# Kernel optimization log

Measured on AMD Instinct MI355X. Metric: run time of the kernel, lower is better.

The kernel has to match this reference:

```python
import jax, jax.numpy as jnp
import numpy as np

T, H = 4096, 2048

def setup_inputs() -> dict:
    key = jax.random.key(0)
    k1, k2, k3 = jax.random.split(key, 3)
    x_sequence = jax.random.normal(k1, (T, H), dtype=jnp.float32)
    lamda = jax.random.normal(k2, (H,), dtype=jnp.float32) * 0.2
    B = jax.random.normal(k3, (H, H), dtype=jnp.float32) / jnp.sqrt(jnp.float32(H))
    return {"x_sequence": x_sequence, "lamda": lamda, "B": B}

def reference(x_sequence, lamda, B):
    # h_t = lamda \odot h_{t-1} + B @ x_t ; initial h_0 = 0 (reset_rtrl_state).
    # Returns stacked h over all T steps, matching torch.stack(outputs).
    def step(h, x_t):
        h_next = lamda * h + B @ x_t  # [H]
        return h_next, h_next
    h0 = jnp.zeros_like(lamda)
    _, hs = jax.lax.scan(step, h0, x_sequence)  # hs: [T, H]
    return hs
```

## Files before the change

kernel.cpp:

```cpp
#include <hip/hip_runtime.h>
#include <hip/hip_bf16.h>

#define T_DIM 4096
#define H_DIM 2048
#define K_DIM 2048
#define NCHUNK 64
#define CLEN 64
#define NT (K_DIM / 64)

typedef float f32x4 __attribute__((ext_vector_type(4)));
typedef _Float16 f16x8 __attribute__((ext_vector_type(8)));

typedef const __attribute__((address_space(1))) char* gp1;
typedef __attribute__((address_space(3))) char* lp3;

static const size_t nX = (size_t)T_DIM * K_DIM;
static const size_t nB = (size_t)H_DIM * K_DIM;

__global__ __launch_bounds__(256) void cvt_swz_all(const float* __restrict__ X,
                                                   const float* __restrict__ Bm,
                                                   _Float16* __restrict__ Xh,
                                                   _Float16* __restrict__ Bh) {
    size_t i = ((size_t)blockIdx.x * 256 + threadIdx.x) * 8;
    const float* in;
    _Float16* out;
    size_t j;
    if (i < nX) { in = X;  out = Xh; j = i; }
    else        { in = Bm; out = Bh; j = i - nX; }
    int row  = (int)(j >> 11);
    int colB = (int)(j & 2047) * 2;
    float a[8];
    *(f32x4*)(a)     = *(const f32x4*)(in + j);
    *(f32x4*)(a + 4) = *(const f32x4*)(in + j + 4);
    f16x8 h;
#pragma unroll
    for (int k = 0; k < 8; ++k) h[k] = (_Float16)a[k];
    size_t ob = (size_t)row * 4096 + (size_t)(colB ^ ((row & 7) << 4));
    *(f16x8*)((char*)out + ob) = h;
}

__global__ __launch_bounds__(512, 4) void gemm_f16(const _Float16* __restrict__ Xh,
                                                   const _Float16* __restrict__ Bh,
                                                   const float* __restrict__ lamda,
                                                   _Float16* __restrict__ Yh,
                                                   float* __restrict__ e) {
    __shared__ __align__(16) _Float16 sMem[2][2][128 * 64];

    int bid = blockIdx.x;
    int swz = (bid & 7) * 64 + (bid >> 3);
    const int h0 = (swz & 15) * 128;
    const int t0 = (swz >> 4) * 128;

    const int tid  = threadIdx.x;
    const int lane = tid & 63;
    const int wave = tid >> 6;
    const int wrow = (wave >> 2) & 1;
    const int wcol = (wave >> 1) & 1;
    const int kks  = wave & 1;
    const int ln15 = lane & 15;
    const int kq   = lane >> 4;

    f32x4 acc[4][4] = {};

    const int srow = tid >> 3;
    const int kcB  = (tid & 7) * 16;
    size_t gA0[2], gB0[2];
    unsigned ldsOff[2];
#pragma unroll
    for (int q = 0; q < 2; ++q) {
        gA0[q] = (size_t)(t0 + srow + q * 64) * 4096 + kcB;
        gB0[q] = (size_t)(h0 + srow + q * 64) * 4096 + kcB;
        ldsOff[q] = (unsigned)(q * 8192 + wave * 1024);
    }

    const int kb = kks * 64 + kq * 16;
    int offA[4], offB[4];
#pragma unroll
    for (int m = 0; m < 4; ++m) {
        int rA = wrow * 64 + m * 16 + ln15;
        offA[m] = rA * 128 + (kb ^ ((rA & 7) << 4));
        int rB = wcol * 64 + m * 16 + ln15;
        offB[m] = rB * 128 + (kb ^ ((rB & 7) << 4));
    }

#define STAGE(buf, kt)                                                                   \
    {                                                                                    \
        _Pragma("unroll")                                                                \
        for (int q = 0; q < 2; ++q) {                                                    \
            __builtin_amdgcn_global_load_lds((gp1)((const char*)Xh + gA0[q] + (kt) * 128), \
                                             (lp3)((char*)sMem[buf][0] + ldsOff[q]), 16, 0, 0); \
            __builtin_amdgcn_global_load_lds((gp1)((const char*)Bh + gB0[q] + (kt) * 128), \
                                             (lp3)((char*)sMem[buf][1] + ldsOff[q]), 16, 0, 0); \
        }                                                                                \
    }

#define COMPUTE(buf)                                                                     \
    {                                                                                    \
        const char* pA = (const char*)sMem[buf][0];                                      \
        const char* pB = (const char*)sMem[buf][1];                                      \
        f16x8 fa[4], fb[4];                                                              \
        _Pragma("unroll")                                                                \
        for (int m = 0; m < 4; ++m) fa[m] = *(const f16x8*)(pA + offA[m]);               \
        _Pragma("unroll")                                                                \
        for (int n = 0; n < 4; ++n) fb[n] = *(const f16x8*)(pB + offB[n]);               \
        _Pragma("unroll")                                                                \
        for (int m = 0; m < 4; ++m)                                                      \
            _Pragma("unroll")                                                            \
            for (int n = 0; n < 4; ++n)                                                  \
                acc[m][n] = __builtin_amdgcn_mfma_f32_16x16x32_f16(fa[m], fb[n],         \
                                                                  acc[m][n], 0, 0, 0);  \
    }

    STAGE(0, 0);
    __syncthreads();

    int cur = 0;
    for (int kt = 0; kt < NT; ++kt) {
        if (kt + 1 < NT) STAGE(cur ^ 1, kt + 1);
        COMPUTE(cur);
        __syncthreads();
        cur ^= 1;
    }
#undef STAGE
#undef COMPUTE

    const int p = wrow * 2 + wcol;
    float* red = (float*)sMem;
    if (kks == 1) {
#pragma unroll
        for (int m = 0; m < 4; ++m)
#pragma unroll
            for (int n = 0; n < 4; ++n)
                *(f32x4*)((char*)red + p * 16384 + (m * 4 + n) * 1024 + lane * 16) = acc[m][n];
    }
    __syncthreads();
    if (kks == 0) {
#pragma unroll
        for (int m = 0; m < 4; ++m)
#pragma unroll
            for (int n = 0; n < 4; ++n)
                acc[m][n] += *(const f32x4*)((const char*)red + p * 16384 + (m * 4 + n) * 1024 + lane * 16);

#pragma unroll
        for (int m = 0; m < 4; ++m) {
            int row = t0 + wrow * 64 + m * 16 + kq * 4;
#pragma unroll
            for (int n = 0; n < 4; ++n) {
                int col = h0 + wcol * 64 + n * 16 + ln15;
#pragma unroll
                for (int j = 0; j < 4; ++j)
                    Yh[(size_t)(row + j) * H_DIM + col] = (_Float16)acc[m][n][j];
            }
        }

        const int c = (t0 >> 6) + wrow;
#pragma unroll
        for (int n = 0; n < 4; ++n) {
            int col = h0 + wcol * 64 + n * 16 + ln15;
            float lam  = lamda[col];
            float lam2 = lam * lam;
            float lam4 = lam2 * lam2;
            float lam16 = lam4 * lam4 * lam4 * lam4;
            float hsum = 0.f;
#pragma unroll
            for (int m = 0; m < 4; ++m) {
                float hm = fmaf(fmaf(fmaf(acc[m][n][0], lam, acc[m][n][1]), lam,
                                     acc[m][n][2]), lam, acc[m][n][3]);
                hsum = fmaf(hsum, lam16, hm);
            }
            float w = 1.f;
            if (kq < 3) w = lam4;
            if (kq < 2) w *= lam4;
            if (kq < 1) w *= lam4;
            float T = hsum * w;
            T += __shfl_xor(T, 16);
            T += __shfl_xor(T, 32);
            if (kq == 0) e[(size_t)c * H_DIM + col] = T;
        }
    }
}

__global__ __launch_bounds__(256) void scanCB(const _Float16* __restrict__ Yh,
                                              float* __restrict__ Y,
                                              const float* __restrict__ lamda,
                                              const float* __restrict__ e) {
    int c = blockIdx.x >> 3;
    int h = (blockIdx.x & 7) * 256 + threadIdx.x;
    float lam = lamda[h];
    float lamL = lam;
#pragma unroll
    for (int i = 0; i < 6; ++i) lamL *= lamL;
    float s = 0.f;
    for (int ci = 0; ci < c; ++ci)
        s = fmaf(lamL, s, e[(size_t)ci * H_DIM + h]);
    const _Float16* qi = Yh + (size_t)c * CLEN * H_DIM + h;
    float* qo = Y + (size_t)c * CLEN * H_DIM + h;
#pragma unroll
    for (int t = 0; t < CLEN; ++t) {
        float v = fmaf(lam, s, (float)qi[(size_t)t * H_DIM]);
        qo[(size_t)t * H_DIM] = v;
        s = v;
    }
}

__global__ __launch_bounds__(256) void gemm_xbT_split(const float* __restrict__ X,
                                                      const float* __restrict__ Bm,
                                                      float* __restrict__ Y) {
    __shared__ __align__(16) _Float16 Ah[128 * 64];
    __shared__ __align__(16) _Float16 Al[128 * 64];
    __shared__ __align__(16) _Float16 Bh2[128 * 64];
    __shared__ __align__(16) _Float16 Bl[128 * 64];

    const int tid  = threadIdx.x;
    const int t0   = blockIdx.y * 128;
    const int h0   = blockIdx.x * 128;
    const int lane = tid & 63;
    const int wave = tid >> 6;
    const int wrow = wave >> 1;
    const int wcol = wave & 1;
    const int ln15 = lane & 15;
    const int kq   = lane >> 4;

    f32x4 acc[4][4] = {};

    int baseA[4], swzA[4], baseB[4], swzB[4];
#pragma unroll
    for (int m = 0; m < 4; ++m) {
        int rA = wrow * 64 + m * 16 + ln15;
        baseA[m] = rA * 128; swzA[m] = (rA & 7) << 4;
        int rB = wcol * 64 + m * 16 + ln15;
        baseB[m] = rB * 128; swzB[m] = (rB & 7) << 4;
    }

    for (int kt = 0; kt < NT; ++kt) {
        const int k0 = kt * 64;
        __syncthreads();
#pragma unroll
        for (int t = 0; t < 4; ++t) {
            int cc  = tid + t * 256;
            int row = cc >> 3;
            int kc  = (cc & 7) * 8;
            size_t gA = (size_t)(t0 + row) * K_DIM + k0 + kc;
            size_t gB = (size_t)(h0 + row) * K_DIM + k0 + kc;
            float a[8], b[8];
            *(float4*)(a)     = *(const float4*)(X + gA);
            *(float4*)(a + 4) = *(const float4*)(X + gA + 4);
            *(float4*)(b)     = *(const float4*)(Bm + gB);
            *(float4*)(b + 4) = *(const float4*)(Bm + gB + 4);
            f16x8 ah, al, bh, bl;
#pragma unroll
            for (int j = 0; j < 8; ++j) {
                _Float16 hh = (_Float16)a[j];
                ah[j] = hh; al[j] = (_Float16)(a[j] - (float)hh);
                _Float16 gg = (_Float16)b[j];
                bh[j] = gg; bl[j] = (_Float16)(b[j] - (float)gg);
            }
            int off = row * 128 + ((kc * 2) ^ ((row & 7) << 4));
            *(f16x8*)((char*)Ah + off)  = ah;
            *(f16x8*)((char*)Al + off)  = al;
            *(f16x8*)((char*)Bh2 + off) = bh;
            *(f16x8*)((char*)Bl + off)  = bl;
        }
        __syncthreads();
#pragma unroll
        for (int kk = 0; kk < 2; ++kk) {
            const int kb2 = kk * 64 + kq * 16;
            f16x8 fa[4], fb[4], ft[4];
#pragma unroll
            for (int m = 0; m < 4; ++m)
                fa[m] = *(const f16x8*)((const char*)Ah + baseA[m] + (kb2 ^ swzA[m]));
#pragma unroll
            for (int m = 0; m < 4; ++m)
                fb[m] = *(const f16x8*)((const char*)Bh2 + baseB[m] + (kb2 ^ swzB[m]));
#pragma unroll
            for (int m = 0; m < 4; ++m)
#pragma unroll
                for (int n = 0; n < 4; ++n)
                    acc[m][n] = __builtin_amdgcn_mfma_f32_16x16x32_f16(fa[m], fb[n], acc[m][n], 0, 0, 0);
#pragma unroll
            for (int m = 0; m < 4; ++m)
                ft[m] = *(const f16x8*)((const char*)Bl + baseB[m] + (kb2 ^ swzB[m]));
#pragma unroll
            for (int m = 0; m < 4; ++m)
#pragma unroll
                for (int n = 0; n < 4; ++n)
                    acc[m][n] = __builtin_amdgcn_mfma_f32_16x16x32_f16(fa[m], ft[n], acc[m][n], 0, 0, 0);
#pragma unroll
            for (int m = 0; m < 4; ++m)
                ft[m] = *(const f16x8*)((const char*)Al + baseA[m] + (kb2 ^ swzA[m]));
#pragma unroll
            for (int m = 0; m < 4; ++m)
#pragma unroll
                for (int n = 0; n < 4; ++n)
                    acc[m][n] = __builtin_amdgcn_mfma_f32_16x16x32_f16(ft[m], fb[n], acc[m][n], 0, 0, 0);
        }
    }

#pragma unroll
    for (int m = 0; m < 4; ++m) {
        int row = t0 + wrow * 64 + m * 16 + kq * 4;
#pragma unroll
        for (int n = 0; n < 4; ++n) {
            int col = h0 + wcol * 64 + n * 16 + ln15;
#pragma unroll
            for (int j = 0; j < 4; ++j)
                Y[(size_t)(row + j) * H_DIM + col] = acc[m][n][j];
        }
    }
}

__global__ __launch_bounds__(256) void scanA(const float* __restrict__ Y,
                                             const float* __restrict__ lamda,
                                             float* __restrict__ e) {
    int c = blockIdx.x >> 3;
    int h = (blockIdx.x & 7) * 256 + threadIdx.x;
    float lam = lamda[h];
    float s = 0.f;
    const float* p = Y + (size_t)c * CLEN * H_DIM + h;
#pragma unroll
    for (int t = 0; t < CLEN; ++t) { s = fmaf(lam, s, *p); p += H_DIM; }
    e[(size_t)c * H_DIM + h] = s;
}

__global__ __launch_bounds__(256) void scanCB_plain(float* __restrict__ Y,
                                                    const float* __restrict__ lamda,
                                                    const float* __restrict__ e) {
    int c = blockIdx.x >> 3;
    int h = (blockIdx.x & 7) * 256 + threadIdx.x;
    float lam = lamda[h];
    float lamL = lam;
#pragma unroll
    for (int i = 0; i < 6; ++i) lamL *= lamL;
    float s = 0.f;
    for (int ci = 0; ci < c; ++ci)
        s = fmaf(lamL, s, e[(size_t)ci * H_DIM + h]);
    float* q = Y + (size_t)c * CLEN * H_DIM + h;
#pragma unroll
    for (int t = 0; t < CLEN; ++t) {
        float v = fmaf(lam, s, q[(size_t)t * H_DIM]);
        q[(size_t)t * H_DIM] = v;
        s = v;
    }
}

extern "C" void kernel_launch(void* const* d_in, const int* in_sizes, int n_in,
                              void* d_out, int out_size, void* d_ws, size_t ws_size,
                              hipStream_t stream) {
    const float* X   = (const float*)d_in[0];
    const float* lam = (const float*)d_in[1];
    const float* Bm  = (const float*)d_in[2];
    float* Y = (float*)d_out;

    const size_t needFused = (2 * nX + nB) * sizeof(_Float16)
                           + (size_t)NCHUNK * H_DIM * sizeof(float);

    if (ws_size >= needFused) {
        _Float16* Xh = (_Float16*)d_ws;
        _Float16* Bh = Xh + nX;
        _Float16* Yh = Bh + nB;
        float* e = (float*)(Yh + nX);

        int cvtBlocks = (int)((nX + nB) / 8 / 256);
        cvt_swz_all<<<dim3(cvtBlocks), 256, 0, stream>>>(X, Bm, Xh, Bh);
        gemm_f16<<<dim3(512), 512, 0, stream>>>(Xh, Bh, lam, Yh, e);
        scanCB<<<dim3(NCHUNK * 8), 256, 0, stream>>>(Yh, Y, lam, e);
    } else {
        dim3 grid(H_DIM / 128, T_DIM / 128);
        gemm_xbT_split<<<grid, 256, 0, stream>>>(X, Bm, Y);
        float* e = (float*)d_ws;
        scanA<<<dim3(NCHUNK * 8), 256, 0, stream>>>(Y, lam, e);
        scanCB_plain<<<dim3(NCHUNK * 8), 256, 0, stream>>>(Y, lam, e);
    }
}
```

Before: 72.94 us.

## Add split-K 256x256-tile GEMM path with dual partial outputs summed in scan

Adds a new GEMM kernel that uses 256x256 output tiles and splits K in two, giving 256 blocks, each writing its own fp16 partial Y and chunk-end state. The scan kernel then sums both partials while it runs the recurrence. Larger tiles raise arithmetic intensity and split-K keeps enough blocks in flight. In exchange it needs extra workspace, writes and reads an additional fp16 Y buffer, and rounds each partial to fp16 before the sum. The old fp32 split fallback path is removed, so small workspaces no longer launch anything.

```diff
diff --git a/kernel.cpp b/kernel.cpp
--- a/kernel.cpp
+++ b/kernel.cpp
@@ -6,7 +6,6 @@
 #define K_DIM 2048
 #define NCHUNK 64
 #define CLEN 64
-#define NT (K_DIM / 64)
 
 typedef float f32x4 __attribute__((ext_vector_type(4)));
 typedef _Float16 f16x8 __attribute__((ext_vector_type(8)));
@@ -39,6 +38,175 @@
     *(f16x8*)((char*)out + ob) = h;
 }
 
+__global__ __launch_bounds__(512, 2) void gemm_sk(const _Float16* __restrict__ Xh,
+                                                  const _Float16* __restrict__ Bh,
+                                                  const float* __restrict__ lamda,
+                                                  _Float16* __restrict__ Yh0,
+                                                  _Float16* __restrict__ Yh1,
+                                                  float* __restrict__ e0,
+                                                  float* __restrict__ e1) {
+    __shared__ __align__(16) _Float16 sA[2][256 * 64];
+    __shared__ __align__(16) _Float16 sB[2][256 * 64];
+
+    const int bid = blockIdx.x;
+    const int x  = bid & 7;
+    const int jj = bid >> 3;
+    const int kz = x >> 2;
+    const int q  = x & 3;
+    const int t0 = (q * 4 + (jj >> 3)) * 256;
+    const int h0 = (jj & 7) * 256;
+    _Float16* __restrict__ Yh = kz ? Yh1 : Yh0;
+    float* __restrict__ e     = kz ? e1 : e0;
+
+    const int tid  = threadIdx.x;
+    const int lane = tid & 63;
+    const int wave = tid >> 6;
+    const int wrow = wave >> 2;
+    const int wcol = wave & 3;
+    const int ln15 = lane & 15;
+    const int kq   = lane >> 4;
+
+    f32x4 acc[8][4] = {};
+
+    size_t gA0[4], gB0[4];
+    unsigned ldsOff[4];
+#pragma unroll
+    for (int t = 0; t < 4; ++t) {
+        int s   = tid + t * 512;
+        int row = s >> 3;
+        int kc  = (s & 7) * 16;
+        gA0[t] = (size_t)(t0 + row) * 4096 + (size_t)(kz * 2048) + kc;
+        gB0[t] = (size_t)(h0 + row) * 4096 + (size_t)(kz * 2048) + kc;
+        ldsOff[t] = (unsigned)((t * 512 + wave * 64) * 16);
+    }
+
+    int baseA[8], swzA[8], baseB[4], swzB[4];
+#pragma unroll
+    for (int m = 0; m < 8; ++m) {
+        int rA = wrow * 128 + m * 16 + ln15;
+        baseA[m] = rA * 128; swzA[m] = (rA & 7) << 4;
+    }
+#pragma unroll
+    for (int n = 0; n < 4; ++n) {
+        int rB = wcol * 64 + n * 16 + ln15;
+        baseB[n] = rB * 128; swzB[n] = (rB & 7) << 4;
+    }
+
+#define STAGE(buf, kt)                                                                   \
+    {                                                                                    \
+        _Pragma("unroll")                                                                \
+        for (int t = 0; t < 4; ++t) {                                                    \
+            __builtin_amdgcn_global_load_lds((gp1)((const char*)Xh + gA0[t] + (kt) * 128), \
+                                             (lp3)((char*)sA[buf] + ldsOff[t]), 16, 0, 0); \
+            __builtin_amdgcn_global_load_lds((gp1)((const char*)Bh + gB0[t] + (kt) * 128), \
+                                             (lp3)((char*)sB[buf] + ldsOff[t]), 16, 0, 0); \
+        }                                                                                \
+    }
+
+#define COMPUTE(buf)                                                                     \
+    {                                                                                    \
+        const char* pA = (const char*)sA[buf];                                           \
+        const char* pB = (const char*)sB[buf];                                           \
+        _Pragma("unroll")                                                                \
+        for (int kk = 0; kk < 2; ++kk) {                                                 \
+            const int kb = kk * 64 + kq * 16;                                            \
+            f16x8 fa[8], fb[4];                                                          \
+            _Pragma("unroll")                                                            \
+            for (int m = 0; m < 8; ++m)                                                  \
+                fa[m] = *(const f16x8*)(pA + baseA[m] + (kb ^ swzA[m]));                 \
+            _Pragma("unroll")                                                            \
+            for (int n = 0; n < 4; ++n)                                                  \
+                fb[n] = *(const f16x8*)(pB + baseB[n] + (kb ^ swzB[n]));                 \
+            _Pragma("unroll")                                                            \
+            for (int m = 0; m < 8; ++m)                                                  \
+                _Pragma("unroll")                                                        \
+                for (int n = 0; n < 4; ++n)                                              \
+                    acc[m][n] = __builtin_amdgcn_mfma_f32_16x16x32_f16(fa[m], fb[n],     \
+                                                                      acc[m][n], 0, 0, 0); \
+        }                                                                                \
+    }
+
+    STAGE(0, 0);
+    __syncthreads();
+
+    int cur = 0;
+    for (int kt = 0; kt < 16; ++kt) {
+        if (kt + 1 < 16) STAGE(cur ^ 1, kt + 1);
+        COMPUTE(cur);
+        __syncthreads();
+        cur ^= 1;
+    }
+#undef STAGE
+#undef COMPUTE
+
+#pragma unroll
+    for (int m = 0; m < 8; ++m) {
+        int row = t0 + wrow * 128 + m * 16 + kq * 4;
+#pragma unroll
+        for (int n = 0; n < 4; ++n) {
+            int col = h0 + wcol * 64 + n * 16 + ln15;
+#pragma unroll
+            for (int j2 = 0; j2 < 4; ++j2)
+                Yh[(size_t)(row + j2) * H_DIM + col] = (_Float16)acc[m][n][j2];
+        }
+    }
+
+#pragma unroll
+    for (int half = 0; half < 2; ++half) {
+        const int c = (t0 >> 6) + wrow * 2 + half;
+#pragma unroll
+        for (int n = 0; n < 4; ++n) {
+            int col = h0 + wcol * 64 + n * 16 + ln15;
+            float lam  = lamda[col];
+            float lam2 = lam * lam;
+            float lam4 = lam2 * lam2;
+            float lam16 = lam4 * lam4 * lam4 * lam4;
+            float hsum = 0.f;
+#pragma unroll
+            for (int mm = 0; mm < 4; ++mm) {
+                int m = half * 4 + mm;
+                float hm = fmaf(fmaf(fmaf(acc[m][n][0], lam, acc[m][n][1]), lam,
+                                     acc[m][n][2]), lam, acc[m][n][3]);
+                hsum = fmaf(hsum, lam16, hm);
+            }
+            float w = 1.f;
+            if (kq < 3) w = lam4;
+            if (kq < 2) w *= lam4;
+            if (kq < 1) w *= lam4;
+            float T = hsum * w;
+            T += __shfl_xor(T, 16);
+            T += __shfl_xor(T, 32);
+            if (kq == 0) e[(size_t)c * H_DIM + col] = T;
+        }
+    }
+}
+
+__global__ __launch_bounds__(256) void scanCB_sk(const _Float16* __restrict__ Yh0,
+                                                 const _Float16* __restrict__ Yh1,
+                                                 float* __restrict__ Y,
+                                                 const float* __restrict__ lamda,
+                                                 const float* __restrict__ e0,
+                                                 const float* __restrict__ e1) {
+    int c = blockIdx.x >> 3;
+    int h = (blockIdx.x & 7) * 256 + threadIdx.x;
+    float lam = lamda[h];
+    float lamL = lam;
+#pragma unroll
+    for (int i = 0; i < 6; ++i) lamL *= lamL;
+    float s = 0.f;
+    for (int ci = 0; ci < c; ++ci)
+        s = fmaf(lamL, s, e0[(size_t)ci * H_DIM + h] + e1[(size_t)ci * H_DIM + h]);
+    const _Float16* q0 = Yh0 + (size_t)c * CLEN * H_DIM + h;
+    const _Float16* q1 = Yh1 + (size_t)c * CLEN * H_DIM + h;
+    float* qo = Y + (size_t)c * CLEN * H_DIM + h;
+#pragma unroll
+    for (int t = 0; t < CLEN; ++t) {
+        float v = fmaf(lam, s, (float)q0[(size_t)t * H_DIM] + (float)q1[(size_t)t * H_DIM]);
+        qo[(size_t)t * H_DIM] = v;
+        s = v;
+    }
+}
+
 __global__ __launch_bounds__(512, 4) void gemm_f16(const _Float16* __restrict__ Xh,
                                                    const _Float16* __restrict__ Bh,
                                                    const float* __restrict__ lamda,
@@ -115,8 +283,8 @@
     __syncthreads();
 
     int cur = 0;
-    for (int kt = 0; kt < NT; ++kt) {
-        if (kt + 1 < NT) STAGE(cur ^ 1, kt + 1);
+    for (int kt = 0; kt < K_DIM / 64; ++kt) {
+        if (kt + 1 < K_DIM / 64) STAGE(cur ^ 1, kt + 1);
         COMPUTE(cur);
         __syncthreads();
         cur ^= 1;
@@ -180,10 +348,10 @@
     }
 }
 
-__global__ __launch_bounds__(256) void scanCB(const _Float16* __restrict__ Yh,
-                                              float* __restrict__ Y,
-                                              const float* __restrict__ lamda,
-                                              const float* __restrict__ e) {
+__global__ __launch_bounds__(256) void scanCB_f16(const _Float16* __restrict__ Yh,
+                                                  float* __restrict__ Y,
+                                                  const float* __restrict__ lamda,
+                                                  const float* __restrict__ e) {
     int c = blockIdx.x >> 3;
     int h = (blockIdx.x & 7) * 256 + threadIdx.x;
     float lam = lamda[h];
@@ -199,146 +367,6 @@
     for (int t = 0; t < CLEN; ++t) {
         float v = fmaf(lam, s, (float)qi[(size_t)t * H_DIM]);
         qo[(size_t)t * H_DIM] = v;
-        s = v;
-    }
-}
-
-__global__ __launch_bounds__(256) void gemm_xbT_split(const float* __restrict__ X,
-                                                      const float* __restrict__ Bm,
-                                                      float* __restrict__ Y) {
-    __shared__ __align__(16) _Float16 Ah[128 * 64];
-    __shared__ __align__(16) _Float16 Al[128 * 64];
-    __shared__ __align__(16) _Float16 Bh2[128 * 64];
-    __shared__ __align__(16) _Float16 Bl[128 * 64];
-
-    const int tid  = threadIdx.x;
-    const int t0   = blockIdx.y * 128;
-    const int h0   = blockIdx.x * 128;
-    const int lane = tid & 63;
-    const int wave = tid >> 6;
-    const int wrow = wave >> 1;
-    const int wcol = wave & 1;
-    const int ln15 = lane & 15;
-    const int kq   = lane >> 4;
-
-    f32x4 acc[4][4] = {};
-
-    int baseA[4], swzA[4], baseB[4], swzB[4];
-#pragma unroll
-    for (int m = 0; m < 4; ++m) {
-        int rA = wrow * 64 + m * 16 + ln15;
-        baseA[m] = rA * 128; swzA[m] = (rA & 7) << 4;
-        int rB = wcol * 64 + m * 16 + ln15;
-        baseB[m] = rB * 128; swzB[m] = (rB & 7) << 4;
-    }
-
-    for (int kt = 0; kt < NT; ++kt) {
-        const int k0 = kt * 64;
-        __syncthreads();
-#pragma unroll
-        for (int t = 0; t < 4; ++t) {
-            int cc  = tid + t * 256;
-            int row = cc >> 3;
-            int kc  = (cc & 7) * 8;
-            size_t gA = (size_t)(t0 + row) * K_DIM + k0 + kc;
-            size_t gB = (size_t)(h0 + row) * K_DIM + k0 + kc;
-            float a[8], b[8];
-            *(float4*)(a)     = *(const float4*)(X + gA);
-            *(float4*)(a + 4) = *(const float4*)(X + gA + 4);
-            *(float4*)(b)     = *(const float4*)(Bm + gB);
-            *(float4*)(b + 4) = *(const float4*)(Bm + gB + 4);
-            f16x8 ah, al, bh, bl;
-#pragma unroll
-            for (int j = 0; j < 8; ++j) {
-                _Float16 hh = (_Float16)a[j];
-                ah[j] = hh; al[j] = (_Float16)(a[j] - (float)hh);
-                _Float16 gg = (_Float16)b[j];
-                bh[j] = gg; bl[j] = (_Float16)(b[j] - (float)gg);
-            }
-            int off = row * 128 + ((kc * 2) ^ ((row & 7) << 4));
-            *(f16x8*)((char*)Ah + off)  = ah;
-            *(f16x8*)((char*)Al + off)  = al;
-            *(f16x8*)((char*)Bh2 + off) = bh;
-            *(f16x8*)((char*)Bl + off)  = bl;
-        }
-        __syncthreads();
-#pragma unroll
-        for (int kk = 0; kk < 2; ++kk) {
-            const int kb2 = kk * 64 + kq * 16;
-            f16x8 fa[4], fb[4], ft[4];
-#pragma unroll
-            for (int m = 0; m < 4; ++m)
-                fa[m] = *(const f16x8*)((const char*)Ah + baseA[m] + (kb2 ^ swzA[m]));
-#pragma unroll
-            for (int m = 0; m < 4; ++m)
-                fb[m] = *(const f16x8*)((const char*)Bh2 + baseB[m] + (kb2 ^ swzB[m]));
-#pragma unroll
-            for (int m = 0; m < 4; ++m)
-#pragma unroll
-                for (int n = 0; n < 4; ++n)
-                    acc[m][n] = __builtin_amdgcn_mfma_f32_16x16x32_f16(fa[m], fb[n], acc[m][n], 0, 0, 0);
-#pragma unroll
-            for (int m = 0; m < 4; ++m)
-                ft[m] = *(const f16x8*)((const char*)Bl + baseB[m] + (kb2 ^ swzB[m]));
-#pragma unroll
-            for (int m = 0; m < 4; ++m)
-#pragma unroll
-                for (int n = 0; n < 4; ++n)
-                    acc[m][n] = __builtin_amdgcn_mfma_f32_16x16x32_f16(fa[m], ft[n], acc[m][n], 0, 0, 0);
-#pragma unroll
-            for (int m = 0; m < 4; ++m)
-                ft[m] = *(const f16x8*)((const char*)Al + baseA[m] + (kb2 ^ swzA[m]));
-#pragma unroll
-            for (int m = 0; m < 4; ++m)
-#pragma unroll
-                for (int n = 0; n < 4; ++n)
-                    acc[m][n] = __builtin_amdgcn_mfma_f32_16x16x32_f16(ft[m], fb[n], acc[m][n], 0, 0, 0);
-        }
-    }
-
-#pragma unroll
-    for (int m = 0; m < 4; ++m) {
-        int row = t0 + wrow * 64 + m * 16 + kq * 4;
-#pragma unroll
-        for (int n = 0; n < 4; ++n) {
-            int col = h0 + wcol * 64 + n * 16 + ln15;
-#pragma unroll
-            for (int j = 0; j < 4; ++j)
-                Y[(size_t)(row + j) * H_DIM + col] = acc[m][n][j];
-        }
-    }
-}
-
-__global__ __launch_bounds__(256) void scanA(const float* __restrict__ Y,
-                                             const float* __restrict__ lamda,
-                                             float* __restrict__ e) {
-    int c = blockIdx.x >> 3;
-    int h = (blockIdx.x & 7) * 256 + threadIdx.x;
-    float lam = lamda[h];
-    float s = 0.f;
-    const float* p = Y + (size_t)c * CLEN * H_DIM + h;
-#pragma unroll
-    for (int t = 0; t < CLEN; ++t) { s = fmaf(lam, s, *p); p += H_DIM; }
-    e[(size_t)c * H_DIM + h] = s;
-}
-
-__global__ __launch_bounds__(256) void scanCB_plain(float* __restrict__ Y,
-                                                    const float* __restrict__ lamda,
-                                                    const float* __restrict__ e) {
-    int c = blockIdx.x >> 3;
-    int h = (blockIdx.x & 7) * 256 + threadIdx.x;
-    float lam = lamda[h];
-    float lamL = lam;
-#pragma unroll
-    for (int i = 0; i < 6; ++i) lamL *= lamL;
-    float s = 0.f;
-    for (int ci = 0; ci < c; ++ci)
-        s = fmaf(lamL, s, e[(size_t)ci * H_DIM + h]);
-    float* q = Y + (size_t)c * CLEN * H_DIM + h;
-#pragma unroll
-    for (int t = 0; t < CLEN; ++t) {
-        float v = fmaf(lam, s, q[(size_t)t * H_DIM]);
-        q[(size_t)t * H_DIM] = v;
         s = v;
     }
 }
@@ -351,24 +379,32 @@
     const float* Bm  = (const float*)d_in[2];
     float* Y = (float*)d_out;
 
-    const size_t needFused = (2 * nX + nB) * sizeof(_Float16)
-                           + (size_t)NCHUNK * H_DIM * sizeof(float);
-
-    if (ws_size >= needFused) {
+    const size_t needSK  = (3 * nX + nB) * sizeof(_Float16)
+                         + 2ull * NCHUNK * H_DIM * sizeof(float);
+    const size_t needR14 = (2 * nX + nB) * sizeof(_Float16)
+                         + (size_t)NCHUNK * H_DIM * sizeof(float);
+
+    int cvtBlocks = (int)((nX + nB) / 8 / 256);
+
+    if (ws_size >= needSK) {
+        _Float16* Xh  = (_Float16*)d_ws;
+        _Float16* Bh  = Xh + nX;
+        _Float16* Yh0 = Bh + nB;
+        _Float16* Yh1 = Yh0 + nX;
+        float* e0 = (float*)(Yh1 + nX);
+        float* e1 = e0 + (size_t)NCHUNK * H_DIM;
+
+        cvt_swz_all<<<dim3(cvtBlocks), 256, 0, stream>>>(X, Bm, Xh, Bh);
+        gemm_sk<<<dim3(256), 512, 0, stream>>>(Xh, Bh, lam, Yh0, Yh1, e0, e1);
+        scanCB_sk<<<dim3(NCHUNK * 8), 256, 0, stream>>>(Yh0, Yh1, Y, lam, e0, e1);
+    } else if (ws_size >= needR14) {
         _Float16* Xh = (_Float16*)d_ws;
         _Float16* Bh = Xh + nX;
         _Float16* Yh = Bh + nB;
         float* e = (float*)(Yh + nX);
 
-        int cvtBlocks = (int)((nX + nB) / 8 / 256);
         cvt_swz_all<<<dim3(cvtBlocks), 256, 0, stream>>>(X, Bm, Xh, Bh);
         gemm_f16<<<dim3(512), 512, 0, stream>>>(Xh, Bh, lam, Yh, e);
-        scanCB<<<dim3(NCHUNK * 8), 256, 0, stream>>>(Yh, Y, lam, e);
-    } else {
-        dim3 grid(H_DIM / 128, T_DIM / 128);
-        gemm_xbT_split<<<grid, 256, 0, stream>>>(X, Bm, Y);
-        float* e = (float*)d_ws;
-        scanA<<<dim3(NCHUNK * 8), 256, 0, stream>>>(Y, lam, e);
-        scanCB_plain<<<dim3(NCHUNK * 8), 256, 0, stream>>>(Y, lam, e);
-    }
-}
+        scanCB_f16<<<dim3(NCHUNK * 8), 256, 0, stream>>>(Yh, Y, lam, e);
+    }
+}
```

Result: slower. 77.28 us (+5.9%).

## Drop split-K waves in f16 GEMM, use 32-wide K tiles with 2x4 wave grid

Applied to the files above, without the earlier changes.

Replaces the intra-block split-K scheme, where wave pairs computed half of each 64-wide K tile and were reduced through LDS, with a 2x4 wave grid in which every wave owns a 64x32 output sub-tile over the full K range. K tiles shrink to 32, which halves LDS use per block, and the launch bound asks for 8 blocks per CU instead of 4. The host-side swizzle in the convert kernel changes to a 4-row XOR within 64-byte groups to match the new LDS layout. The tail LDS reduction and its extra barrier go away, but there are twice as many K iterations, each with a barrier, and each wave now does less MFMA work per fragment it loads.

```diff
diff --git a/kernel.cpp b/kernel.cpp
--- a/kernel.cpp
+++ b/kernel.cpp
@@ -6,7 +6,7 @@
 #define K_DIM 2048
 #define NCHUNK 64
 #define CLEN 64
-#define NT (K_DIM / 64)
+#define NT32 (K_DIM / 32)
 
 typedef float f32x4 __attribute__((ext_vector_type(4)));
 typedef _Float16 f16x8 __attribute__((ext_vector_type(8)));
@@ -35,16 +35,18 @@
     f16x8 h;
 #pragma unroll
     for (int k = 0; k < 8; ++k) h[k] = (_Float16)a[k];
-    size_t ob = (size_t)row * 4096 + (size_t)(colB ^ ((row & 7) << 4));
+    unsigned sw = (unsigned)(colB & ~63) | (((unsigned)colB & 63u) ^ (((unsigned)row & 3u) << 4));
+    size_t ob = (size_t)row * 4096 + sw;
     *(f16x8*)((char*)out + ob) = h;
 }
 
-__global__ __launch_bounds__(512, 4) void gemm_f16(const _Float16* __restrict__ Xh,
+__global__ __launch_bounds__(512, 8) void gemm_f16(const _Float16* __restrict__ Xh,
                                                    const _Float16* __restrict__ Bh,
                                                    const float* __restrict__ lamda,
                                                    _Float16* __restrict__ Yh,
                                                    float* __restrict__ e) {
-    __shared__ __align__(16) _Float16 sMem[2][2][128 * 64];
+    __shared__ __align__(16) _Float16 sA[2][128 * 32];
+    __shared__ __align__(16) _Float16 sB[2][128 * 32];
 
     int bid = blockIdx.x;
     int swz = (bid & 7) * 64 + (bid >> 3);
@@ -54,59 +56,52 @@
     const int tid  = threadIdx.x;
     const int lane = tid & 63;
     const int wave = tid >> 6;
-    const int wrow = (wave >> 2) & 1;
-    const int wcol = (wave >> 1) & 1;
-    const int kks  = wave & 1;
+    const int wrow = wave >> 2;
+    const int wcol = wave & 3;
     const int ln15 = lane & 15;
     const int kq   = lane >> 4;
 
-    f32x4 acc[4][4] = {};
-
-    const int srow = tid >> 3;
-    const int kcB  = (tid & 7) * 16;
-    size_t gA0[2], gB0[2];
-    unsigned ldsOff[2];
-#pragma unroll
-    for (int q = 0; q < 2; ++q) {
-        gA0[q] = (size_t)(t0 + srow + q * 64) * 4096 + kcB;
-        gB0[q] = (size_t)(h0 + srow + q * 64) * 4096 + kcB;
-        ldsOff[q] = (unsigned)(q * 8192 + wave * 1024);
-    }
-
-    const int kb = kks * 64 + kq * 16;
-    int offA[4], offB[4];
+    f32x4 acc[4][2] = {};
+
+    const int srow = tid >> 2;
+    const int kcB  = (tid & 3) * 16;
+    const size_t gA0 = (size_t)(t0 + srow) * 4096 + kcB;
+    const size_t gB0 = (size_t)(h0 + srow) * 4096 + kcB;
+    const unsigned ldsOff = (unsigned)(wave * 1024);
+
+    int offA[4], offB[2];
 #pragma unroll
     for (int m = 0; m < 4; ++m) {
         int rA = wrow * 64 + m * 16 + ln15;
-        offA[m] = rA * 128 + (kb ^ ((rA & 7) << 4));
-        int rB = wcol * 64 + m * 16 + ln15;
-        offB[m] = rB * 128 + (kb ^ ((rB & 7) << 4));
+        offA[m] = rA * 64 + ((kq * 16) ^ ((rA & 3) << 4));
+    }
+#pragma unroll
+    for (int n = 0; n < 2; ++n) {
+        int rB = wcol * 32 + n * 16 + ln15;
+        offB[n] = rB * 64 + ((kq * 16) ^ ((rB & 3) << 4));
     }
 
 #define STAGE(buf, kt)                                                                   \
     {                                                                                    \
-        _Pragma("unroll")                                                                \
-        for (int q = 0; q < 2; ++q) {                                                    \
-            __builtin_amdgcn_global_load_lds((gp1)((const char*)Xh + gA0[q] + (kt) * 128), \
-                                             (lp3)((char*)sMem[buf][0] + ldsOff[q]), 16, 0, 0); \
-            __builtin_amdgcn_global_load_lds((gp1)((const char*)Bh + gB0[q] + (kt) * 128), \
-                                             (lp3)((char*)sMem[buf][1] + ldsOff[q]), 16, 0, 0); \
-        }                                                                                \
+        __builtin_amdgcn_global_load_lds((gp1)((const char*)Xh + gA0 + (kt) * 64),       \
+                                         (lp3)((char*)sA[buf] + ldsOff), 16, 0, 0);      \
+        __builtin_amdgcn_global_load_lds((gp1)((const char*)Bh + gB0 + (kt) * 64),       \
+                                         (lp3)((char*)sB[buf] + ldsOff), 16, 0, 0);      \
     }
 
 #define COMPUTE(buf)                                                                     \
     {                                                                                    \
-        const char* pA = (const char*)sMem[buf][0];                                      \
-        const char* pB = (const char*)sMem[buf][1];                                      \
-        f16x8 fa[4], fb[4];                                                              \
+        const char* pA = (const char*)sA[buf];                                           \
+        const char* pB = (const char*)sB[buf];                                           \
+        f16x8 fa[4], fb[2];                                                              \
         _Pragma("unroll")                                                                \
         for (int m = 0; m < 4; ++m) fa[m] = *(const f16x8*)(pA + offA[m]);               \
         _Pragma("unroll")                                                                \
-        for (int n = 0; n < 4; ++n) fb[n] = *(const f16x8*)(pB + offB[n]);               \
+        for (int n = 0; n < 2; ++n) fb[n] = *(const f16x8*)(pB + offB[n]);               \
         _Pragma("unroll")                                                                \
         for (int m = 0; m < 4; ++m)                                                      \
             _Pragma("unroll")                                                            \
-            for (int n = 0; n < 4; ++n)                                                  \
+            for (int n = 0; n < 2; ++n)                                                  \
                 acc[m][n] = __builtin_amdgcn_mfma_f32_16x16x32_f16(fa[m], fb[n],         \
                                                                   acc[m][n], 0, 0, 0);  \
     }
@@ -115,8 +110,8 @@
     __syncthreads();
 
     int cur = 0;
-    for (int kt = 0; kt < NT; ++kt) {
-        if (kt + 1 < NT) STAGE(cur ^ 1, kt + 1);
+    for (int kt = 0; kt < NT32; ++kt) {
+        if (kt + 1 < NT32) STAGE(cur ^ 1, kt + 1);
         COMPUTE(cur);
         __syncthreads();
         cur ^= 1;
@@ -124,59 +119,41 @@
 #undef STAGE
 #undef COMPUTE
 
-    const int p = wrow * 2 + wcol;
-    float* red = (float*)sMem;
-    if (kks == 1) {
-#pragma unroll
-        for (int m = 0; m < 4; ++m)
-#pragma unroll
-            for (int n = 0; n < 4; ++n)
-                *(f32x4*)((char*)red + p * 16384 + (m * 4 + n) * 1024 + lane * 16) = acc[m][n];
-    }
-    __syncthreads();
-    if (kks == 0) {
-#pragma unroll
-        for (int m = 0; m < 4; ++m)
-#pragma unroll
-            for (int n = 0; n < 4; ++n)
-                acc[m][n] += *(const f32x4*)((const char*)red + p * 16384 + (m * 4 + n) * 1024 + lane * 16);
-
+#pragma unroll
+    for (int m = 0; m < 4; ++m) {
+        int row = t0 + wrow * 64 + m * 16 + kq * 4;
+#pragma unroll
+        for (int n = 0; n < 2; ++n) {
+            int col = h0 + wcol * 32 + n * 16 + ln15;
+#pragma unroll
+            for (int j = 0; j < 4; ++j)
+                Yh[(size_t)(row + j) * H_DIM + col] = (_Float16)acc[m][n][j];
+        }
+    }
+
+    const int c = (t0 >> 6) + wrow;
+#pragma unroll
+    for (int n = 0; n < 2; ++n) {
+        int col = h0 + wcol * 32 + n * 16 + ln15;
+        float lam  = lamda[col];
+        float lam2 = lam * lam;
+        float lam4 = lam2 * lam2;
+        float lam16 = lam4 * lam4 * lam4 * lam4;
+        float hsum = 0.f;
 #pragma unroll
         for (int m = 0; m < 4; ++m) {
-            int row = t0 + wrow * 64 + m * 16 + kq * 4;
-#pragma unroll
-            for (int n = 0; n < 4; ++n) {
-                int col = h0 + wcol * 64 + n * 16 + ln15;
-#pragma unroll
-                for (int j = 0; j < 4; ++j)
-                    Yh[(size_t)(row + j) * H_DIM + col] = (_Float16)acc[m][n][j];
-            }
-        }
-
-        const int c = (t0 >> 6) + wrow;
-#pragma unroll
-        for (int n = 0; n < 4; ++n) {
-            int col = h0 + wcol * 64 + n * 16 + ln15;
-            float lam  = lamda[col];
-            float lam2 = lam * lam;
-            float lam4 = lam2 * lam2;
-            float lam16 = lam4 * lam4 * lam4 * lam4;
-            float hsum = 0.f;
-#pragma unroll
-            for (int m = 0; m < 4; ++m) {
-                float hm = fmaf(fmaf(fmaf(acc[m][n][0], lam, acc[m][n][1]), lam,
-                                     acc[m][n][2]), lam, acc[m][n][3]);
-                hsum = fmaf(hsum, lam16, hm);
-            }
-            float w = 1.f;
-            if (kq < 3) w = lam4;
-            if (kq < 2) w *= lam4;
-            if (kq < 1) w *= lam4;
-            float T = hsum * w;
-            T += __shfl_xor(T, 16);
-            T += __shfl_xor(T, 32);
-            if (kq == 0) e[(size_t)c * H_DIM + col] = T;
-        }
+            float hm = fmaf(fmaf(fmaf(acc[m][n][0], lam, acc[m][n][1]), lam,
+                                 acc[m][n][2]), lam, acc[m][n][3]);
+            hsum = fmaf(hsum, lam16, hm);
+        }
+        float w = 1.f;
+        if (kq < 3) w = lam4;
+        if (kq < 2) w *= lam4;
+        if (kq < 1) w *= lam4;
+        float T = hsum * w;
+        T += __shfl_xor(T, 16);
+        T += __shfl_xor(T, 32);
+        if (kq == 0) e[(size_t)c * H_DIM + col] = T;
     }
 }
 
@@ -232,7 +209,7 @@
         baseB[m] = rB * 128; swzB[m] = (rB & 7) << 4;
     }
 
-    for (int kt = 0; kt < NT; ++kt) {
+    for (int kt = 0; kt < K_DIM / 64; ++kt) {
         const int k0 = kt * 64;
         __syncthreads();
 #pragma unroll
```

Measured after the change: 85.24 us. 16.9% more time.
